# Kernel optimization log

Hardware: AMD Instinct MI355X
Metric: run time of the kernel (lower is better)

The kernel has to match this reference:

```python
import jax, jax.numpy as jnp
import numpy as np

EPS = 1e-6  # torch.nn.PairwiseDistance default eps, added to the difference


def setup_inputs() -> dict:
    key = jax.random.key(0)
    latents = jax.random.normal(key, (16384, 64, 1, 1), dtype=jnp.float32)
    return {"latents": latents}


def reference(latents) -> jnp.ndarray:
    n = latents.shape[0]
    v = latents.squeeze(-1).squeeze(-1)            # [N, D]
    dp = v @ v.T                                   # [N, N]
    dp = dp.at[jnp.diag_indices(n)].set(-1.0)      # exclude self-match
    idx = jnp.argmax(dp, axis=1)                   # nearest neighbor by dot product
    # PairwiseDistance(p=2): ||x1 - x2 + eps||_2
    dist = jnp.linalg.norm(v - v[idx] + EPS, axis=1)  # [N]
    koleo = -jnp.log(dist * n)
    koleo = jnp.where(koleo < 0, jnp.zeros_like(koleo), koleo)
    return koleo.mean()
```

## Files before the change

kernel.cpp:

```cpp
#include <hip/hip_runtime.h>
#include <math.h>

#define N_PTS 16384
#define DIM   64

typedef short short8 __attribute__((ext_vector_type(8)));
typedef float f32x4  __attribute__((ext_vector_type(4)));

constexpr int TPB     = 512;
constexpr int MI      = 2;
constexpr int CHUNK   = 256;
constexpr int NCH     = N_PTS / CHUNK;
constexpr int NBLK    = NCH * (NCH + 1) / 2;
constexpr int NT      = CHUNK / 16;
constexpr int BSTRIDE = DIM + 8;
constexpr int CSTR4   = 256;

constexpr float    BIAS    = 2048.0f;
constexpr unsigned KEYMASK = 0xFFFFC000u;

__device__ __forceinline__ unsigned max3u(unsigned a, unsigned b, unsigned c) {
    return max(max(a, b), c);
}

__device__ __forceinline__ unsigned rowmax16(unsigned k) {
    unsigned r;
    r = (unsigned)__builtin_amdgcn_update_dpp(0, (int)k, 0x121, 0xF, 0xF, true); k = max(k, r);
    r = (unsigned)__builtin_amdgcn_update_dpp(0, (int)k, 0x122, 0xF, 0xF, true); k = max(k, r);
    r = (unsigned)__builtin_amdgcn_update_dpp(0, (int)k, 0x124, 0xF, 0xF, true); k = max(k, r);
    r = (unsigned)__builtin_amdgcn_update_dpp(0, (int)k, 0x128, 0xF, 0xF, true); k = max(k, r);
    return k;
}

__device__ __forceinline__ short8 pack8(float4 a, float4 b) {
    union { unsigned u[4]; short8 s; } r;
    r.u[0] = __builtin_amdgcn_perm(__float_as_uint(a.y), __float_as_uint(a.x), 0x07060302);
    r.u[1] = __builtin_amdgcn_perm(__float_as_uint(a.w), __float_as_uint(a.z), 0x07060302);
    r.u[2] = __builtin_amdgcn_perm(__float_as_uint(b.y), __float_as_uint(b.x), 0x07060302);
    r.u[3] = __builtin_amdgcn_perm(__float_as_uint(b.w), __float_as_uint(b.z), 0x07060302);
    return r.s;
}

__global__ __launch_bounds__(256) void to_bf16(const float* __restrict__ vf,
                                               unsigned short* __restrict__ vb) {
    const int i = blockIdx.x * 256 + threadIdx.x;
    const float4* s = (const float4*)(vf + (size_t)i * 8);
    *(short8*)(vb + (size_t)i * 8) = pack8(s[0], s[1]);
}

template<bool BSRC16>
__global__ __launch_bounds__(TPB) void argmax_mfma(const float* __restrict__ vf,
                                                   const unsigned short* __restrict__ vb,
                                                   int* __restrict__ best,
                                                   float* __restrict__ acc,
                                                   unsigned* __restrict__ cnt) {
    __shared__ unsigned short smB[CHUNK * BSTRIDE];
    __shared__ unsigned       colmax4[4 * CSTR4];

    const int b = blockIdx.x;
    int ib = (int)((129.0f - sqrtf(16641.0f - 8.0f * (float)b)) * 0.5f);
    while ((64 * (ib + 1) - ((ib + 1) * ib) / 2) <= b) ++ib;
    while ((64 * ib - (ib * (ib - 1)) / 2) > b) --ib;
    const int  jch  = ib + (b - (64 * ib - (ib * (ib - 1)) / 2));
    const bool diag = (ib == jch);
    const int  rb0  = ib  * CHUNK;
    const int  cb0  = jch * CHUNK;

    const int t     = threadIdx.x;
    const int wave  = t >> 6;
    const int lane  = t & 63;
    const int col16 = lane & 15;
    const int quad  = lane >> 4;

    colmax4[t] = 0u;
    colmax4[512 + t] = 0u;

    if (b == 0 && t == 0) { *acc = 0.0f; *cnt = 0u; }

#pragma unroll
    for (int w = 0; w < 4; ++w) {
        const int s   = t + w * 512;
        const int row = s >> 3;
        const int k8  = s & 7;
        if constexpr (BSRC16) {
            *(short8*)&smB[row * BSTRIDE + k8 * 8] =
                *(const short8*)(vb + (size_t)(cb0 + row) * DIM + k8 * 8);
        } else {
            const float4* src = (const float4*)(vf + (size_t)(cb0 + row) * DIM + k8 * 8);
            *(short8*)&smB[row * BSTRIDE + k8 * 8] = pack8(src[0], src[1]);
        }
    }

    const int wave_row0 = rb0 + wave * 32;
    const int loc_row0  = wave * 32;

    short8 a0[MI], a1[MI];
#pragma unroll
    for (int mi = 0; mi < MI; ++mi) {
        if constexpr (BSRC16) {
            const unsigned short* ap = vb + (size_t)(wave_row0 + mi * 16 + col16) * DIM + quad * 8;
            a0[mi] = *(const short8*)(ap);
            a1[mi] = *(const short8*)(ap + 32);
        } else {
            const float4* ap = (const float4*)(vf + (size_t)(wave_row0 + mi * 16 + col16) * DIM + quad * 8);
            a0[mi] = pack8(ap[0], ap[1]);
            a1[mi] = pack8(ap[8], ap[9]);
        }
    }

    unsigned bk[MI][4];
#pragma unroll
    for (int mi = 0; mi < MI; ++mi)
#pragma unroll
        for (int r = 0; r < 4; ++r) bk[mi][r] = 0u;

    unsigned cmk[NT];
#pragma unroll
    for (int tt = 0; tt < NT; ++tt) cmk[tt] = 0u;

    const f32x4 cinit = {BIAS, BIAS, BIAS, BIAS};

    __syncthreads();

    const unsigned short* bl0 = &smB[col16 * BSTRIDE + quad * 8];
    unsigned* cmbase = &colmax4[quad * CSTR4 + col16];
    short8 b0 = *(const short8*)(bl0);
    short8 b1 = *(const short8*)(bl0 + 32);

#pragma unroll
    for (int tt = 0; tt < NT; ++tt) {
        const int tn = (tt + 1) & (NT - 1);
        const unsigned short* bln = bl0 + tn * 16 * BSTRIDE;
        short8 nb0 = *(const short8*)(bln);
        short8 nb1 = *(const short8*)(bln + 32);

        f32x4 ac[MI];
#pragma unroll
        for (int mi = 0; mi < MI; ++mi) {
            ac[mi] = __builtin_amdgcn_mfma_f32_16x16x32_bf16(a0[mi], b0, cinit, 0, 0, 0);
            ac[mi] = __builtin_amdgcn_mfma_f32_16x16x32_bf16(a1[mi], b1, ac[mi], 0, 0, 0);
        }

        const int      jb   = cb0 + tt * 16;
        const unsigned jcol = (unsigned)(jb + col16);

#pragma unroll
        for (int mi = 0; mi < MI; ++mi) {
            const int rb = wave_row0 + mi * 16;
            if (diag && rb == jb) {
#pragma unroll
                for (int r = 0; r < 4; ++r) {
                    unsigned key = (__float_as_uint(ac[mi][r]) & KEYMASK) | jcol;
                    if (col16 == quad * 4 + r) key = 0u;
                    bk[mi][r] = max(bk[mi][r], key);
                }
            } else {
#pragma unroll
                for (int r = 0; r < 4; ++r) {
                    unsigned key = (__float_as_uint(ac[mi][r]) & KEYMASK) | jcol;
                    bk[mi][r] = max(bk[mi][r], key);
                }
            }
        }

        if (!diag) {
            unsigned ck[MI * 4];
#pragma unroll
            for (int mi = 0; mi < MI; ++mi)
#pragma unroll
                for (int r = 0; r < 4; ++r)
                    ck[mi * 4 + r] = (__float_as_uint(ac[mi][r]) & KEYMASK)
                                   | (unsigned)(loc_row0 + mi * 16 + quad * 4 + r);
            cmk[tt] = max3u(max3u(ck[0], ck[1], ck[2]),
                            max3u(ck[3], ck[4], ck[5]),
                            max(ck[6], ck[7]));
        }

        b0 = nb0; b1 = nb1;
    }

#pragma unroll
    for (int mi = 0; mi < MI; ++mi) {
#pragma unroll
        for (int r = 0; r < 4; ++r) {
            const unsigned k0 = rowmax16(bk[mi][r]);
            if (col16 == 0) {
                const int row = wave_row0 + mi * 16 + quad * 4 + r;
                atomicMax(&best[row], (int)k0);
            }
        }
    }

    if (!diag) {
#pragma unroll
        for (int tt = 0; tt < NT; ++tt)
            atomicMax(cmbase + tt * 16, cmk[tt]);
    }

    if (!diag) {
        __syncthreads();
        if (t < CHUNK) {
            const unsigned k = max3u(max(colmax4[t], colmax4[CSTR4 + t]),
                                     colmax4[2 * CSTR4 + t],
                                     colmax4[3 * CSTR4 + t]);
            atomicMax(&best[cb0 + t], (int)(k + (unsigned)rb0));
        }
    }
}

__global__ __launch_bounds__(256) void koleo_kernel(const float* __restrict__ v,
                                                    const int* __restrict__ best,
                                                    float* __restrict__ acc,
                                                    unsigned* __restrict__ cnt,
                                                    float* __restrict__ out) {
    const int i = blockIdx.x * blockDim.x + threadIdx.x;
    const unsigned j = ((unsigned)best[i]) & 0x3FFFu;
    float s = 0.f;
#pragma unroll
    for (int k = 0; k < 16; ++k) {
        float4 a = ((const float4*)(v + (size_t)i * DIM))[k];
        float4 b = ((const float4*)(v + (size_t)j * DIM))[k];
        float dx = a.x - b.x + 1e-6f;
        float dy = a.y - b.y + 1e-6f;
        float dz = a.z - b.z + 1e-6f;
        float dw = a.w - b.w + 1e-6f;
        s += dx * dx + dy * dy + dz * dz + dw * dw;
    }
    float dist = sqrtf(s);
    float kol  = -logf(dist * (float)N_PTS);
    if (kol < 0.f) kol = 0.f;
#pragma unroll
    for (int off = 32; off > 0; off >>= 1) kol += __shfl_down(kol, off);
    if ((threadIdx.x & 63) == 0) atomicAdd(acc, kol);

    __syncthreads();
    if (threadIdx.x == 0) {
        __threadfence();
        unsigned old = atomicAdd(cnt, 1u);
        if (old == gridDim.x - 1) {
            __threadfence();
            float total = atomicAdd(acc, 0.0f);
            out[0] = total / (float)N_PTS;
        }
    }
}

extern "C" void kernel_launch(void* const* d_in, const int* in_sizes, int n_in,
                              void* d_out, int out_size, void* d_ws, size_t ws_size,
                              hipStream_t stream) {
    const float* v   = (const float*)d_in[0];
    float*       out = (float*)d_out;

    int*      best = (int*)d_ws;
    float*    acc  = (float*)((char*)d_ws + (size_t)N_PTS * 4);
    unsigned* cnt  = (unsigned*)(acc + 1);
    unsigned short* vb = (unsigned short*)((char*)d_ws + (size_t)N_PTS * 4 + 256);
    const size_t need = (size_t)N_PTS * 4 + 256 + (size_t)N_PTS * DIM * 2;

    if (ws_size >= need) {
        to_bf16<<<N_PTS * DIM / (256 * 8), 256, 0, stream>>>(v, vb);
        argmax_mfma<true><<<NBLK, TPB, 0, stream>>>(v, vb, best, acc, cnt);
    } else {
        argmax_mfma<false><<<NBLK, TPB, 0, stream>>>(v, (const unsigned short*)nullptr,
                                                     best, acc, cnt);
    }
    koleo_kernel<<<N_PTS / 256, 256, 0, stream>>>(v, best, acc, cnt, out);
}
```

Measured before the change: 98.49 us.

## Exploit symmetry within diagonal tiles and pair two diagonal chunks per block

Diagonal 256x256 tiles previously computed the full square and used only row maxima. Now each diagonal block handles two diagonal chunks and computes only the upper-triangular 16x16 subtiles, using the column reduction to cover the mirrored half. Waves are assigned in reverse order in the second phase to balance the triangular work. B fragments are read directly from global memory, and the column-max accumulation in the off-diagonal path now uses per-iteration LDS atomics instead of register arrays. This removes redundant MFMA work and lowers the diagonal block count, but adds more LDS atomics, a variable-length loop and global-load latency in the diagonal path.

```diff
diff --git a/kernel.cpp b/kernel.cpp
--- a/kernel.cpp
+++ b/kernel.cpp
@@ -11,10 +11,13 @@
 constexpr int MI      = 2;
 constexpr int CHUNK   = 256;
 constexpr int NCH     = N_PTS / CHUNK;
-constexpr int NBLK    = NCH * (NCH + 1) / 2;
+constexpr int NDIAG   = NCH / 2;
+constexpr int NOFF    = NCH * (NCH - 1) / 2;
+constexpr int NBLK    = NDIAG + NOFF;
 constexpr int NT      = CHUNK / 16;
 constexpr int BSTRIDE = DIM + 8;
 constexpr int CSTR4   = 256;
+
 
 constexpr float    BIAS    = 2048.0f;
 constexpr unsigned KEYMASK = 0xFFFFC000u;
@@ -54,28 +57,150 @@
                                                    int* __restrict__ best,
                                                    float* __restrict__ acc,
                                                    unsigned* __restrict__ cnt) {
-    __shared__ unsigned short smB[CHUNK * BSTRIDE];
-    __shared__ unsigned       colmax4[4 * CSTR4];
-
-    const int b = blockIdx.x;
-    int ib = (int)((129.0f - sqrtf(16641.0f - 8.0f * (float)b)) * 0.5f);
-    while ((64 * (ib + 1) - ((ib + 1) * ib) / 2) <= b) ++ib;
-    while ((64 * ib - (ib * (ib - 1)) / 2) > b) --ib;
-    const int  jch  = ib + (b - (64 * ib - (ib * (ib - 1)) / 2));
-    const bool diag = (ib == jch);
-    const int  rb0  = ib  * CHUNK;
-    const int  cb0  = jch * CHUNK;
-
+    __shared__ __align__(16) unsigned char shraw[CHUNK * BSTRIDE * 2 + 4 * CSTR4 * 4];
+    unsigned short* smB     = (unsigned short*)shraw;
+    unsigned*       colmax4 = (unsigned*)(shraw + CHUNK * BSTRIDE * 2);
+    unsigned*       colD    = (unsigned*)shraw;
+
+    const int b     = blockIdx.x;
     const int t     = threadIdx.x;
     const int wave  = t >> 6;
     const int lane  = t & 63;
     const int col16 = lane & 15;
     const int quad  = lane >> 4;
 
+    if (b == 0 && t == 0) { *acc = 0.0f; *cnt = 0u; }
+
+    const f32x4 cinit = {BIAS, BIAS, BIAS, BIAS};
+
+    if (b < NDIAG) {
+        colD[t] = 0u; colD[512 + t] = 0u; colD[1024 + t] = 0u; colD[1536 + t] = 0u;
+        __syncthreads();
+
+#pragma unroll
+        for (int ph = 0; ph < 2; ++ph) {
+            const int c  = 2 * b + ph;
+            const int g  = ph ? (7 - wave) : wave;
+            const int rloc0 = g * 32;
+
+            short8 a0[MI], a1[MI];
+#pragma unroll
+            for (int mi = 0; mi < MI; ++mi) {
+                if constexpr (BSRC16) {
+                    const unsigned short* ap = vb +
+                        (size_t)(c * CHUNK + rloc0 + mi * 16 + col16) * DIM + quad * 8;
+                    a0[mi] = *(const short8*)(ap);
+                    a1[mi] = *(const short8*)(ap + 32);
+                } else {
+                    const float4* ap = (const float4*)(vf +
+                        (size_t)(c * CHUNK + rloc0 + mi * 16 + col16) * DIM + quad * 8);
+                    a0[mi] = pack8(ap[0], ap[1]);
+                    a1[mi] = pack8(ap[8], ap[9]);
+                }
+            }
+
+            unsigned bk[MI][4];
+#pragma unroll
+            for (int mi = 0; mi < MI; ++mi)
+#pragma unroll
+                for (int r = 0; r < 4; ++r) bk[mi][r] = 0u;
+
+            const int t0 = 2 * g;
+
+            short8 cb0, cb1;
+            if constexpr (BSRC16) {
+                const unsigned short* bp = vb +
+                    (size_t)(c * CHUNK + t0 * 16 + col16) * DIM + quad * 8;
+                cb0 = *(const short8*)(bp);
+                cb1 = *(const short8*)(bp + 32);
+            } else {
+                const float4* bp = (const float4*)(vf +
+                    (size_t)(c * CHUNK + t0 * 16 + col16) * DIM + quad * 8);
+                cb0 = pack8(bp[0], bp[1]);
+                cb1 = pack8(bp[8], bp[9]);
+            }
+
+            for (int tt = t0; tt < NT; ++tt) {
+                const int tn = (tt + 1 < NT) ? tt + 1 : t0;
+                short8 nb0, nb1;
+                if constexpr (BSRC16) {
+                    const unsigned short* bp = vb +
+                        (size_t)(c * CHUNK + tn * 16 + col16) * DIM + quad * 8;
+                    nb0 = *(const short8*)(bp);
+                    nb1 = *(const short8*)(bp + 32);
+                } else {
+                    const float4* bp = (const float4*)(vf +
+                        (size_t)(c * CHUNK + tn * 16 + col16) * DIM + quad * 8);
+                    nb0 = pack8(bp[0], bp[1]);
+                    nb1 = pack8(bp[8], bp[9]);
+                }
+
+                f32x4 ac[MI];
+#pragma unroll
+                for (int mi = 0; mi < MI; ++mi) {
+                    ac[mi] = __builtin_amdgcn_mfma_f32_16x16x32_bf16(a0[mi], cb0, cinit, 0, 0, 0);
+                    ac[mi] = __builtin_amdgcn_mfma_f32_16x16x32_bf16(a1[mi], cb1, ac[mi], 0, 0, 0);
+                }
+
+                const unsigned jcol = (unsigned)(c * CHUNK + tt * 16 + col16);
+
+                unsigned ck[MI * 4];
+#pragma unroll
+                for (int mi = 0; mi < MI; ++mi) {
+                    const bool selft = (tt == 2 * g + mi);
+#pragma unroll
+                    for (int r = 0; r < 4; ++r) {
+                        const bool self = selft && (col16 == quad * 4 + r);
+                        unsigned vbits  = __float_as_uint(ac[mi][r]) & KEYMASK;
+                        unsigned rkey   = self ? 0u : (vbits | jcol);
+                        bk[mi][r] = max(bk[mi][r], rkey);
+                        ck[mi * 4 + r] = self ? 0u :
+                            (vbits | (unsigned)(rloc0 + mi * 16 + quad * 4 + r));
+                    }
+                }
+                const unsigned mt = max3u(max3u(ck[0], ck[1], ck[2]),
+                                          max3u(ck[3], ck[4], ck[5]),
+                                          max(ck[6], ck[7]));
+                atomicMax(&colD[ph * 1024 + quad * CSTR4 + tt * 16 + col16], mt);
+
+                cb0 = nb0; cb1 = nb1;
+            }
+
+#pragma unroll
+            for (int mi = 0; mi < MI; ++mi) {
+#pragma unroll
+                for (int r = 0; r < 4; ++r) {
+                    const unsigned k0 = rowmax16(bk[mi][r]);
+                    if (col16 == 0) {
+                        const int row = c * CHUNK + rloc0 + mi * 16 + quad * 4 + r;
+                        atomicMax(&best[row], (int)k0);
+                    }
+                }
+            }
+        }
+
+        __syncthreads();
+        {
+            const int ph = t >> 8, cc = t & 255, c = 2 * b + ph;
+            const unsigned k = max3u(max(colD[ph * 1024 + cc],
+                                         colD[ph * 1024 + CSTR4 + cc]),
+                                     colD[ph * 1024 + 2 * CSTR4 + cc],
+                                     colD[ph * 1024 + 3 * CSTR4 + cc]);
+            atomicMax(&best[c * CHUNK + cc], (int)(k + (unsigned)(c * CHUNK)));
+        }
+        return;
+    }
+
+    const int b2 = b - NDIAG;
+    int ib = (int)((127.0f - sqrtf(16129.0f - 8.0f * (float)b2)) * 0.5f);
+    while (63 * (ib + 1) - ((ib + 1) * ib) / 2 <= b2) ++ib;
+    while (63 * ib - (ib * (ib - 1)) / 2 > b2) --ib;
+    const int jch = ib + 1 + (b2 - (63 * ib - (ib * (ib - 1)) / 2));
+    const int rb0 = ib  * CHUNK;
+    const int cb0 = jch * CHUNK;
+
     colmax4[t] = 0u;
     colmax4[512 + t] = 0u;
-
-    if (b == 0 && t == 0) { *acc = 0.0f; *cnt = 0u; }
 
 #pragma unroll
     for (int w = 0; w < 4; ++w) {
@@ -114,12 +239,6 @@
 #pragma unroll
         for (int r = 0; r < 4; ++r) bk[mi][r] = 0u;
 
-    unsigned cmk[NT];
-#pragma unroll
-    for (int tt = 0; tt < NT; ++tt) cmk[tt] = 0u;
-
-    const f32x4 cinit = {BIAS, BIAS, BIAS, BIAS};
-
     __syncthreads();
 
     const unsigned short* bl0 = &smB[col16 * BSTRIDE + quad * 8];
@@ -141,40 +260,21 @@
             ac[mi] = __builtin_amdgcn_mfma_f32_16x16x32_bf16(a1[mi], b1, ac[mi], 0, 0, 0);
         }
 
-        const int      jb   = cb0 + tt * 16;
-        const unsigned jcol = (unsigned)(jb + col16);
-
-#pragma unroll
-        for (int mi = 0; mi < MI; ++mi) {
-            const int rb = wave_row0 + mi * 16;
-            if (diag && rb == jb) {
-#pragma unroll
-                for (int r = 0; r < 4; ++r) {
-                    unsigned key = (__float_as_uint(ac[mi][r]) & KEYMASK) | jcol;
-                    if (col16 == quad * 4 + r) key = 0u;
-                    bk[mi][r] = max(bk[mi][r], key);
-                }
-            } else {
-#pragma unroll
-                for (int r = 0; r < 4; ++r) {
-                    unsigned key = (__float_as_uint(ac[mi][r]) & KEYMASK) | jcol;
-                    bk[mi][r] = max(bk[mi][r], key);
-                }
-            }
-        }
-
-        if (!diag) {
-            unsigned ck[MI * 4];
-#pragma unroll
-            for (int mi = 0; mi < MI; ++mi)
-#pragma unroll
-                for (int r = 0; r < 4; ++r)
-                    ck[mi * 4 + r] = (__float_as_uint(ac[mi][r]) & KEYMASK)
-                                   | (unsigned)(loc_row0 + mi * 16 + quad * 4 + r);
-            cmk[tt] = max3u(max3u(ck[0], ck[1], ck[2]),
-                            max3u(ck[3], ck[4], ck[5]),
-                            max(ck[6], ck[7]));
-        }
+        const unsigned jcol = (unsigned)(cb0 + tt * 16 + col16);
+
+        unsigned ck[MI * 4];
+#pragma unroll
+        for (int mi = 0; mi < MI; ++mi)
+#pragma unroll
+            for (int r = 0; r < 4; ++r) {
+                const unsigned vbits = __float_as_uint(ac[mi][r]) & KEYMASK;
+                bk[mi][r] = max(bk[mi][r], vbits | jcol);
+                ck[mi * 4 + r] = vbits | (unsigned)(loc_row0 + mi * 16 + quad * 4 + r);
+            }
+        const unsigned mt = max3u(max3u(ck[0], ck[1], ck[2]),
+                                  max3u(ck[3], ck[4], ck[5]),
+                                  max(ck[6], ck[7]));
+        atomicMax(cmbase + tt * 16, mt);
 
         b0 = nb0; b1 = nb1;
     }
@@ -191,20 +291,12 @@
         }
     }
 
-    if (!diag) {
-#pragma unroll
-        for (int tt = 0; tt < NT; ++tt)
-            atomicMax(cmbase + tt * 16, cmk[tt]);
-    }
-
-    if (!diag) {
-        __syncthreads();
-        if (t < CHUNK) {
-            const unsigned k = max3u(max(colmax4[t], colmax4[CSTR4 + t]),
-                                     colmax4[2 * CSTR4 + t],
-                                     colmax4[3 * CSTR4 + t]);
-            atomicMax(&best[cb0 + t], (int)(k + (unsigned)rb0));
-        }
+    __syncthreads();
+    if (t < CHUNK) {
+        const unsigned k = max3u(max(colmax4[t], colmax4[CSTR4 + t]),
+                                 colmax4[2 * CSTR4 + t],
+                                 colmax4[3 * CSTR4 + t]);
+        atomicMax(&best[cb0 + t], (int)(k + (unsigned)rb0));
     }
 }
 
```

New measurement: 112.6 us. 1.14x slower.

## Retile waves as 4x2 grid with 64 rows by 128 columns each

Applied to the files above, without the earlier changes.

Changes each wave's tile from 32 rows across all 256 columns to 64 rows (four MFMA row tiles) across half the columns, arranged as a 4x2 wave grid. Each B fragment loaded from LDS is now reused across four A tiles instead of two, which halves LDS reads per MFMA. Column-max atomics to shared memory are issued inside the loop instead of being buffered in registers, and the B prefetch is dropped. The cost is more A registers per wave and an LDS atomic in every iteration.

```diff
diff --git a/kernel.cpp b/kernel.cpp
--- a/kernel.cpp
+++ b/kernel.cpp
@@ -8,13 +8,14 @@
 typedef float f32x4  __attribute__((ext_vector_type(4)));
 
 constexpr int TPB     = 512;
-constexpr int MI      = 2;
+constexpr int MI      = 4;
 constexpr int CHUNK   = 256;
 constexpr int NCH     = N_PTS / CHUNK;
 constexpr int NBLK    = NCH * (NCH + 1) / 2;
-constexpr int NT      = CHUNK / 16;
+constexpr int NTW     = 8;
 constexpr int BSTRIDE = DIM + 8;
 constexpr int CSTR4   = 256;
+
 
 constexpr float    BIAS    = 2048.0f;
 constexpr unsigned KEYMASK = 0xFFFFC000u;
@@ -68,6 +69,8 @@
 
     const int t     = threadIdx.x;
     const int wave  = t >> 6;
+    const int wr    = wave >> 1;
+    const int wc    = wave & 1;
     const int lane  = t & 63;
     const int col16 = lane & 15;
     const int quad  = lane >> 4;
@@ -91,8 +94,8 @@
         }
     }
 
-    const int wave_row0 = rb0 + wave * 32;
-    const int loc_row0  = wave * 32;
+    const int wave_row0 = rb0 + wr * 64;
+    const int loc_row0  = wr * 64;
 
     short8 a0[MI], a1[MI];
 #pragma unroll
@@ -114,25 +117,18 @@
 #pragma unroll
         for (int r = 0; r < 4; ++r) bk[mi][r] = 0u;
 
-    unsigned cmk[NT];
-#pragma unroll
-    for (int tt = 0; tt < NT; ++tt) cmk[tt] = 0u;
-
     const f32x4 cinit = {BIAS, BIAS, BIAS, BIAS};
 
     __syncthreads();
 
-    const unsigned short* bl0 = &smB[col16 * BSTRIDE + quad * 8];
-    unsigned* cmbase = &colmax4[quad * CSTR4 + col16];
-    short8 b0 = *(const short8*)(bl0);
-    short8 b1 = *(const short8*)(bl0 + 32);
-
-#pragma unroll
-    for (int tt = 0; tt < NT; ++tt) {
-        const int tn = (tt + 1) & (NT - 1);
-        const unsigned short* bln = bl0 + tn * 16 * BSTRIDE;
-        short8 nb0 = *(const short8*)(bln);
-        short8 nb1 = *(const short8*)(bln + 32);
+    const unsigned short* blw = &smB[(wc * 128 + col16) * BSTRIDE + quad * 8];
+    unsigned* cmbase = &colmax4[quad * CSTR4 + wc * 128 + col16];
+
+#pragma unroll
+    for (int tt = 0; tt < NTW; ++tt) {
+        const unsigned short* bp = blw + tt * 16 * BSTRIDE;
+        const short8 b0 = *(const short8*)(bp);
+        const short8 b1 = *(const short8*)(bp + 32);
 
         f32x4 ac[MI];
 #pragma unroll
@@ -141,7 +137,7 @@
             ac[mi] = __builtin_amdgcn_mfma_f32_16x16x32_bf16(a1[mi], b1, ac[mi], 0, 0, 0);
         }
 
-        const int      jb   = cb0 + tt * 16;
+        const int      jb   = cb0 + wc * 128 + tt * 16;
         const unsigned jcol = (unsigned)(jb + col16);
 
 #pragma unroll
@@ -164,19 +160,22 @@
         }
 
         if (!diag) {
-            unsigned ck[MI * 4];
-#pragma unroll
-            for (int mi = 0; mi < MI; ++mi)
-#pragma unroll
-                for (int r = 0; r < 4; ++r)
-                    ck[mi * 4 + r] = (__float_as_uint(ac[mi][r]) & KEYMASK)
-                                   | (unsigned)(loc_row0 + mi * 16 + quad * 4 + r);
-            cmk[tt] = max3u(max3u(ck[0], ck[1], ck[2]),
-                            max3u(ck[3], ck[4], ck[5]),
-                            max(ck[6], ck[7]));
-        }
-
-        b0 = nb0; b1 = nb1;
+            unsigned pm[MI];
+#pragma unroll
+            for (int mi = 0; mi < MI; ++mi) {
+                unsigned k0 = (__float_as_uint(ac[mi][0]) & KEYMASK)
+                            | (unsigned)(loc_row0 + mi * 16 + quad * 4 + 0);
+                unsigned k1 = (__float_as_uint(ac[mi][1]) & KEYMASK)
+                            | (unsigned)(loc_row0 + mi * 16 + quad * 4 + 1);
+                unsigned k2 = (__float_as_uint(ac[mi][2]) & KEYMASK)
+                            | (unsigned)(loc_row0 + mi * 16 + quad * 4 + 2);
+                unsigned k3 = (__float_as_uint(ac[mi][3]) & KEYMASK)
+                            | (unsigned)(loc_row0 + mi * 16 + quad * 4 + 3);
+                pm[mi] = max(max3u(k0, k1, k2), k3);
+            }
+            const unsigned mt = max(max3u(pm[0], pm[1], pm[2]), pm[3]);
+            atomicMax(cmbase + tt * 16, mt);
+        }
     }
 
 #pragma unroll
@@ -189,12 +188,6 @@
                 atomicMax(&best[row], (int)k0);
             }
         }
-    }
-
-    if (!diag) {
-#pragma unroll
-        for (int tt = 0; tt < NT; ++tt)
-            atomicMax(cmbase + tt * 16, cmk[tt]);
     }
 
     if (!diag) {
```

Measured after the change: 114.2 us. +16.0%, slower.
